# Performance work log

Hardware: AMD Instinct MI355X
Metric: run time of the kernel (lower is better)

## Reference

```python
import jax, jax.numpy as jnp
import numpy as np

BLANK = 0
B, T, D_TN = 32, 1000, 640
D_PN, D_J, V = 640, 640, 1024


def lstm_step(x, h, c, W_ih, W_hh, b):
    # x:[B,D_PN] h,c:[B,D_PN]
    gates = x @ W_ih.T + h @ W_hh.T + b  # [B,4*D_PN]
    i, f, g, o = jnp.split(gates, 4, axis=-1)
    c_new = jax.nn.sigmoid(f) * c + jax.nn.sigmoid(i) * jnp.tanh(g)
    h_new = jax.nn.sigmoid(o) * jnp.tanh(c_new)
    return h_new, c_new


def setup_inputs() -> dict:
    key = jax.random.key(0)
    ks = jax.random.split(key, 10)
    s_pn = 1.0 / np.sqrt(D_PN)
    s_tn = 1.0 / np.sqrt(D_TN)
    s_j = 1.0 / np.sqrt(D_J)
    return {
        "tn_output": jax.random.normal(ks[0], (B, T, D_TN), jnp.float32),
        "E": jax.random.normal(ks[1], (V, D_PN), jnp.float32) * 0.02,
        "W_ih": jax.random.normal(ks[2], (4 * D_PN, D_PN), jnp.float32) * s_pn,
        "W_hh": jax.random.normal(ks[3], (4 * D_PN, D_PN), jnp.float32) * s_pn,
        "b_lstm": jnp.zeros((4 * D_PN,), jnp.float32),
        "W_tn": jax.random.normal(ks[4], (D_J, D_TN), jnp.float32) * s_tn,
        "W_pn": jax.random.normal(ks[5], (D_J, D_PN), jnp.float32) * s_pn,
        "b_joint": jnp.zeros((D_J,), jnp.float32),
        "W_out": jax.random.normal(ks[6], (V, D_J), jnp.float32) * s_j,
        "b_out": jnp.zeros((V,), jnp.float32),
    }


def reference(tn_output, E, W_ih, W_hh, b_lstm, W_tn, W_pn, b_joint, W_out, b_out):
    """Vectorized transducer greedy decode (beam_size=1 path).
    Returns (emitted_tokens [B,T] (blank where no emission), logp_scores [B],
    mean exp score scalar) mirroring the torch module's greedy output."""
    b, t = tn_output.shape[0], tn_output.shape[1]
    dt = tn_output.dtype
    # initial PN step on initial_token_id (= blank), hidden None -> zeros
    h0 = jnp.zeros((b, W_hh.shape[1]), dt)
    c0 = jnp.zeros((b, W_hh.shape[1]), dt)
    x0 = E[jnp.full((b,), BLANK)]
    h, c = lstm_step(x0, h0, c0, W_ih, W_hh, b_lstm)
    out_pn = h
    # precompute TN projection for the whole utterance: [T,B,D_J]
    tn_proj = jnp.einsum("btd,jd->tbj", tn_output, W_tn)

    def step(state, tn_t):
        h, c, out_pn, last_tok, score = state
        z = jnp.tanh(tn_t + out_pn @ W_pn.T + b_joint)          # [B,D_J]
        logp = jax.nn.log_softmax(z @ W_out.T + b_out, axis=-1)  # [B,V]
        pos = jnp.argmax(logp, axis=-1).astype(jnp.int32)        # [B]
        lp = jnp.take_along_axis(logp, pos[:, None].astype(jnp.int32), axis=-1)[:, 0]
        nonblank = pos != BLANK
        score = score + jnp.where(nonblank, lp, jnp.zeros_like(lp))
        tok = jnp.where(nonblank, pos, last_tok)
        # PN advances only for hyps that emitted a non-blank label
        h2, c2 = lstm_step(E[tok], h, c, W_ih, W_hh, b_lstm)
        m = nonblank[:, None]
        h_n = jnp.where(m, h2, h)
        c_n = jnp.where(m, c2, c)
        out_n = jnp.where(m, h2, out_pn)
        emit = jnp.where(nonblank, pos, jnp.full_like(pos, BLANK))
        return (h_n, c_n, out_n, tok, score), emit

    init = (h, c, out_pn, jnp.full((b,), BLANK, jnp.int32), jnp.zeros((b,), dt))
    (_, _, _, _, score), emits = jax.lax.scan(step, init, tn_proj)
    tokens = jnp.swapaxes(emits, 0, 1)  # [B,T]
    return tokens, score, jnp.exp(score).mean()
```

## Files before the change

### kernel.cpp

```cpp
#include <hip/hip_runtime.h>
#include <stdint.h>


typedef unsigned long long u64;
typedef uint32_t u32;

#define TT 1000
#define DD 640
#define GG 2560
#define VV 1024

#define NA 80
#define NL 64
#define NC 80
#define NBLK (NA + NL + NC)

static constexpr size_t OFF_WTN  = 0;
static constexpr size_t OFF_WPN  = OFF_WTN  + 409600;
static constexpr size_t OFF_WHH  = OFF_WPN  + 409600;
static constexpr size_t OFF_WOUT = OFF_WHH  + 1638400;
static constexpr size_t OFF_P    = OFF_WOUT + 655360;
static constexpr size_t OFF_XH   = OFF_P    + 2621440;
static constexpr size_t OFF_XZ   = OFF_XH   + 40960;
static constexpr size_t OFF_SC   = OFF_XZ   + 20480;
static constexpr size_t OFF_LKEY = OFF_SC   + 32;
static constexpr size_t OFF_LSE  = OFF_LKEY + 4096;
static constexpr size_t OFF_FA   = OFF_LSE  + 2048;
static constexpr size_t OFF_FL   = OFF_FA   + 2560;
static constexpr size_t OFF_FC   = OFF_FL   + 2048;
static constexpr size_t OFF_EP   = OFF_FC   + 2560;
static constexpr size_t OFF_END  = OFF_EP   + 96;

__device__ __forceinline__ float sigf(float x) { return 1.0f / (1.0f + expf(-x)); }

__device__ __forceinline__ u32 ordf(float f) {
  u32 u = __float_as_uint(f);
  return (u & 0x80000000u) ? ~u : (u | 0x80000000u);
}

__device__ __forceinline__ void cstore2(float* p, float a, float b) {
  u64 v = ((u64)__float_as_uint(b) << 32) | (u64)__float_as_uint(a);
  __hip_atomic_store((u64*)p, v, __ATOMIC_RELAXED, __HIP_MEMORY_SCOPE_AGENT);
}
__device__ __forceinline__ float2 cload2(const float* p) {
  u64 v = __hip_atomic_load((const u64*)p, __ATOMIC_RELAXED, __HIP_MEMORY_SCOPE_AGENT);
  return make_float2(__uint_as_float((u32)v), __uint_as_float((u32)(v >> 32)));
}
__device__ __forceinline__ u64 cloadu64(const u64* p) {
  return __hip_atomic_load(p, __ATOMIC_RELAXED, __HIP_MEMORY_SCOPE_AGENT);
}
__device__ __forceinline__ void cstoreu64(u64* p, u64 v) {
  __hip_atomic_store(p, v, __ATOMIC_RELAXED, __HIP_MEMORY_SCOPE_AGENT);
}
__device__ __forceinline__ float cloadf(const float* p) {
  return __hip_atomic_load(p, __ATOMIC_RELAXED, __HIP_MEMORY_SCOPE_AGENT);
}
__device__ __forceinline__ void cstoref(float* p, float v) {
  __hip_atomic_store(p, v, __ATOMIC_RELAXED, __HIP_MEMORY_SCOPE_AGENT);
}

__device__ __forceinline__ void poll_flags(const int* F, int n, int target) {
  if ((int)threadIdx.x < n) {
    while (__hip_atomic_load(F + threadIdx.x * 32, __ATOMIC_RELAXED,
                             __HIP_MEMORY_SCOPE_AGENT) < target)
      __builtin_amdgcn_s_sleep(1);
  }
  __syncthreads();
}
__device__ __forceinline__ void poll1(const int* ep, int target) {
  if (threadIdx.x == 0) {
    while (__hip_atomic_load(ep, __ATOMIC_RELAXED, __HIP_MEMORY_SCOPE_AGENT) < target)
      __builtin_amdgcn_s_sleep(1);
  }
  __syncthreads();
}
__device__ __forceinline__ void set_flag(int* F, int idx, int val) {
  __syncthreads();
  if (threadIdx.x == 0)
    __hip_atomic_store(F + idx * 32, val, __ATOMIC_RELAXED, __HIP_MEMORY_SCOPE_AGENT);
}

__device__ __forceinline__ void fma4(float& a, const float4 w, const float4 x) {
  a = fmaf(w.x, x.x, fmaf(w.y, x.y, fmaf(w.z, x.z, fmaf(w.w, x.w, a))));
}
__device__ __forceinline__ void fma22(float& a, const float4 w, const float2 xa,
                                      const float2 xb) {
  a = fmaf(w.x, xa.x, fmaf(w.y, xa.y, fmaf(w.z, xb.x, fmaf(w.w, xb.y, a))));
}


__global__ __launch_bounds__(256) void k_wt4(const float* __restrict__ W,
                                             float* __restrict__ WT4, int J) {
  __shared__ float tile[64][65];
  int nj = J >> 6;
  int tj = blockIdx.x % nj, tk = blockIdx.x / nj;
  int jb = tj << 6, kb = tk << 6;
  for (int i = threadIdx.x; i < 4096; i += 256) {
    int d = i & 63, j = i >> 6;
    tile[j][d] = W[(size_t)(jb + j) * DD + (kb + d)];
  }
  __syncthreads();
  for (int i = threadIdx.x; i < 1024; i += 256) {
    int j = i & 63, q = i >> 6;
    float4 v = make_float4(tile[j][q * 4], tile[j][q * 4 + 1], tile[j][q * 4 + 2],
                           tile[j][q * 4 + 3]);
    ((float4*)WT4)[(size_t)((kb >> 2) + q) * J + (jb + j)] = v;
  }
}

__global__ __launch_bounds__(256) void k_pgemm(const float* __restrict__ E,
                                               const float* __restrict__ Wih,
                                               float* __restrict__ P) {
  __shared__ float As[16][65], Bs[16][65];
  int vt = blockIdx.x & 15, gt = blockIdx.x >> 4;
  int vb = vt << 6, gb = gt << 6;
  int tv = threadIdx.x & 15, tg = threadIdx.x >> 4;
  float acc[4][4] = {};
  for (int kb = 0; kb < DD; kb += 16) {
    for (int i = threadIdx.x; i < 1024; i += 256) {
      int k = i & 15, x = i >> 4;
      As[k][x] = E[(size_t)(vb + x) * DD + kb + k];
      Bs[k][x] = Wih[(size_t)(gb + x) * DD + kb + k];
    }
    __syncthreads();
#pragma unroll
    for (int k = 0; k < 16; ++k) {
      float av[4], bv[4];
#pragma unroll
      for (int i = 0; i < 4; ++i) av[i] = As[k][tv * 4 + i];
#pragma unroll
      for (int j = 0; j < 4; ++j) bv[j] = Bs[k][tg * 4 + j];
#pragma unroll
      for (int i = 0; i < 4; ++i)
#pragma unroll
        for (int j = 0; j < 4; ++j) acc[i][j] = fmaf(av[i], bv[j], acc[i][j]);
    }
    __syncthreads();
  }
#pragma unroll
  for (int i = 0; i < 4; ++i)
#pragma unroll
    for (int j = 0; j < 4; ++j)
      P[(size_t)(vb + tv * 4 + i) * GG + gb + tg * 4 + j] = acc[i][j];
}

__global__ __launch_bounds__(256) void k_init(float* __restrict__ ws,
                                              const float* __restrict__ bl) {
  const float* P = ws + OFF_P;
  float* XH0 = ws + OFF_XH;
  int tid = blockIdx.x * 256 + threadIdx.x;
  if (tid < DD) {
    int j = tid;
    float gi = P[j] + bl[j];
    float gg = P[1280 + j] + bl[1280 + j];
    float go = P[1920 + j] + bl[1920 + j];
    float c1 = sigf(gi) * tanhf(gg);
    float h1 = sigf(go) * tanhf(c1);
    for (int b = 0; b < 32; ++b) XH0[b * DD + j] = h1;
  }
  if (blockIdx.x == 3) {
    int* FA = (int*)(ws + OFF_FA);
    int* FL = (int*)(ws + OFF_FL);
    int* FC = (int*)(ws + OFF_FC);
    int* EP = (int*)(ws + OFF_EP);
    for (int i = threadIdx.x; i < 224; i += 256) {
      int* p = (i < 80) ? (FA + i * 32)
                        : (i < 144) ? (FL + (i - 80) * 32) : (FC + (i - 144) * 32);
      *p = 0;
    }
    if (threadIdx.x < 3) EP[threadIdx.x * 32] = 0;
  }
}

__global__ __launch_bounds__(256, 1) void k_decode(float* __restrict__ ws,
                                                   const float* __restrict__ tn,
                                                   const float* __restrict__ bl,
                                                   const float* __restrict__ bj,
                                                   const float* __restrict__ bo,
                                                   float* __restrict__ out) {
  const float* WTN = ws + OFF_WTN;
  const float* WPN = ws + OFF_WPN;
  const float* WHH = ws + OFF_WHH;
  const float* WOUT = ws + OFF_WOUT;
  const float* P = ws + OFF_P;
  float* XH = ws + OFF_XH;
  float* XZ = ws + OFF_XZ;
  float* SCg = ws + OFF_SC;
  u64* LKEY = (u64*)(ws + OFF_LKEY);
  float* LSE = ws + OFF_LSE;
  int* FA = (int*)(ws + OFF_FA);
  int* FL = (int*)(ws + OFF_FL);
  int* FC = (int*)(ws + OFF_FC);
  int* EFC = (int*)(ws + OFF_EP) + 0;
  int* EFA = (int*)(ws + OFF_EP) + 32;
  int* EFL = (int*)(ws + OFF_EP) + 64;

  __shared__ float xbuf[32 * 648];
  __shared__ float red[16 * 16 * 33];
  __shared__ float aux[32 * 33];
  __shared__ u64 kred[32 * 9];
  __shared__ float sered[32 * 9];
  __shared__ float c_lds[8 * 33], h_lds[8 * 33];
  __shared__ float sc_lds[32];
  __shared__ int tok_lds[32], nb_lds[32], lt_lds[32];

  const int bid = blockIdx.x, tid = threadIdx.x;
  const int dq = tid >> 4, bp = tid & 15;
  const int d0 = dq * 40, b0 = bp * 2;

  if (bid < NA) {
    const int j0 = bid * 8;
    for (int t = 0; t < TT; ++t) {
      const int par = t & 1;
      float acc[8][2] = {};
      const float* t0p = tn + ((size_t)b0 * TT + t) * DD + d0;
      const float* t1p = t0p + (size_t)TT * DD;
#pragma unroll 5
      for (int q = 0; q < 10; ++q) {
        float4 x0 = *(const float4*)(t0p + q * 4);
        float4 x1 = *(const float4*)(t1p + q * 4);
        const float4* wt = (const float4*)WTN + (size_t)((d0 + q * 4) >> 2) * DD + j0;
#pragma unroll
        for (int r = 0; r < 8; ++r) {
          fma4(acc[r][0], wt[r], x0);
          fma4(acc[r][1], wt[r], x1);
        }
      }
      if (bid == 0) {
        poll_flags(FC, NC, t);
        if (tid == 0)
          __hip_atomic_store(EFC, t, __ATOMIC_RELAXED, __HIP_MEMORY_SCOPE_AGENT);
      } else {
        poll1(EFC, t);
      }
      const float* h0p = XH + (size_t)par * 20480 + (size_t)b0 * DD + d0;
      const float* h1p = h0p + DD;
#pragma unroll 5
      for (int q = 0; q < 10; ++q) {
        float2 a0 = cload2(h0p + q * 4), a1 = cload2(h0p + q * 4 + 2);
        float2 b1 = cload2(h1p + q * 4), b2 = cload2(h1p + q * 4 + 2);
        const float4* wp = (const float4*)WPN + (size_t)((d0 + q * 4) >> 2) * DD + j0;
#pragma unroll
        for (int r = 0; r < 8; ++r) {
          fma22(acc[r][0], wp[r], a0, a1);
          fma22(acc[r][1], wp[r], b1, b2);
        }
      }
#pragma unroll
      for (int r = 0; r < 8; ++r) {
        red[(dq * 8 + r) * 33 + b0] = acc[r][0];
        red[(dq * 8 + r) * 33 + b0 + 1] = acc[r][1];
      }
      __syncthreads();
      {
        int r = tid >> 5, b = tid & 31;
        float s = 0.f;
#pragma unroll
        for (int k = 0; k < 16; ++k) s += red[(k * 8 + r) * 33 + b];
        aux[r * 33 + b] = tanhf(s + bj[j0 + r]);
      }
      __syncthreads();
      if (tid < 128) {
        int jp = tid >> 5, b = tid & 31;
        cstore2(XZ + (size_t)b * DD + j0 + jp * 2, aux[(jp * 2) * 33 + b],
                aux[(jp * 2 + 1) * 33 + b]);
      }
      set_flag(FA, bid, t + 1);
    }
  } else if (bid < NA + NL) {
    const int lb = bid - NA, v0 = lb * 16;
    for (int t = 0; t < TT; ++t) {
      if (lb == 0) {
        poll_flags(FA, NA, t + 1);
        if (tid == 0)
          __hip_atomic_store(EFA, t + 1, __ATOMIC_RELAXED, __HIP_MEMORY_SCOPE_AGENT);
      } else {
        poll1(EFA, t + 1);
      }
      const float* z0p = XZ + (size_t)b0 * DD + d0;
      const float* z1p = z0p + DD;
      float acc[16][2] = {};
#pragma unroll 5
      for (int q = 0; q < 10; ++q) {
        float2 z0a = cload2(z0p + q * 4), z0b = cload2(z0p + q * 4 + 2);
        float2 z1a = cload2(z1p + q * 4), z1b = cload2(z1p + q * 4 + 2);
        const float4* wo = (const float4*)WOUT + (size_t)((d0 + q * 4) >> 2) * VV + v0;
#pragma unroll
        for (int r = 0; r < 16; ++r) {
          float4 w = wo[r];
          fma22(acc[r][0], w, z0a, z0b);
          fma22(acc[r][1], w, z1a, z1b);
        }
      }
#pragma unroll
      for (int r = 0; r < 16; ++r) {
        red[(dq * 16 + r) * 33 + b0] = acc[r][0];
        red[(dq * 16 + r) * 33 + b0 + 1] = acc[r][1];
      }
      __syncthreads();
#pragma unroll
      for (int o = tid; o < 512; o += 256) {
        int r = o >> 5, b = o & 31;
        float s = bo[v0 + r];
#pragma unroll
        for (int k = 0; k < 16; ++k) s += red[(k * 16 + r) * 33 + b];
        aux[r * 33 + b] = s;
      }
      __syncthreads();
      if (tid < 32) {
        int b = tid;
        float m = -1e30f, se = 0.f;
        int vbest = 0;
#pragma unroll
        for (int r = 0; r < 16; ++r) {
          float x = aux[r * 33 + b];
          se += expf(x);
          if (x > m) { m = x; vbest = r; }
        }
        u64 key = ((u64)ordf(m) << 32) | (u64)(0xFFFFFFFFu - (u32)(v0 + vbest));
        cstoreu64(&LKEY[(size_t)b * 64 + lb], key);
        cstoref(&LSE[(size_t)b * 64 + lb], se);
      }
      set_flag(FL, lb, t + 1);
    }
  } else {
    const int cb = bid - (NA + NL), j0 = cb * 8;
    {
      int jj = tid >> 5, b = tid & 31, j = j0 + jj;
      float gi = P[j] + bl[j];
      float gg = P[1280 + j] + bl[1280 + j];
      float go = P[1920 + j] + bl[1920 + j];
      float c1 = sigf(gi) * tanhf(gg);
      c_lds[jj * 33 + b] = c1;
      h_lds[jj * 33 + b] = sigf(go) * tanhf(c1);
    }
    if (tid < 32) { lt_lds[tid] = 0; sc_lds[tid] = 0.f; }
    __syncthreads();
    for (int t = 0; t < TT; ++t) {
      const int par = t & 1;
      poll1(EFC, t);
      {
        const float* h0p = XH + (size_t)par * 20480 + (size_t)b0 * DD + d0;
        const float* h1p = h0p + DD;
#pragma unroll 5
        for (int q = 0; q < 10; ++q) {
          float2 a0 = cload2(h0p + q * 4), a1 = cload2(h0p + q * 4 + 2);
          float2 b1 = cload2(h1p + q * 4), b2 = cload2(h1p + q * 4 + 2);
          *(float4*)&xbuf[b0 * 648 + d0 + q * 4] = make_float4(a0.x, a0.y, a1.x, a1.y);
          *(float4*)&xbuf[(b0 + 1) * 648 + d0 + q * 4] = make_float4(b1.x, b1.y, b2.x, b2.y);
        }
      }
      __syncthreads();
#pragma unroll
      for (int p = 0; p < 2; ++p) {
        float acc[16][2] = {};
#pragma unroll 5
        for (int q = 0; q < 10; ++q) {
          const int d = d0 + q * 4;
          float4 h0 = *(const float4*)&xbuf[b0 * 648 + d];
          float4 h1 = *(const float4*)&xbuf[(b0 + 1) * 648 + d];
          const float4* wa =
              (const float4*)WHH + (size_t)(d >> 2) * GG + (2 * p) * DD + j0;
          const float4* wb = wa + DD;
#pragma unroll
          for (int jj = 0; jj < 8; ++jj) {
            fma4(acc[jj][0], wa[jj], h0);
            fma4(acc[jj][1], wa[jj], h1);
            fma4(acc[8 + jj][0], wb[jj], h0);
            fma4(acc[8 + jj][1], wb[jj], h1);
          }
        }
#pragma unroll
        for (int r = 0; r < 16; ++r) {
          red[(dq * 16 + r) * 33 + b0] = acc[r][0];
          red[(dq * 16 + r) * 33 + b0 + 1] = acc[r][1];
        }
        __syncthreads();
#pragma unroll
        for (int o = tid; o < 512; o += 256) {
          int r16 = o >> 5, b = o & 31;
          float s = 0.f;
#pragma unroll
          for (int k = 0; k < 16; ++k) s += red[(k * 16 + r16) * 33 + b];
          int g = 2 * p + (r16 >> 3), jj = r16 & 7;
          aux[(g * 8 + jj) * 33 + b] = s;
        }
        __syncthreads();
      }
      if (cb == 0) {
        poll_flags(FL, NL, t + 1);
        if (tid == 0)
          __hip_atomic_store(EFL, t + 1, __ATOMIC_RELAXED, __HIP_MEMORY_SCOPE_AGENT);
      } else {
        poll1(EFL, t + 1);
      }
      {
        int b = tid >> 3, ch = tid & 7;
        const u64* kp = LKEY + (size_t)b * 64 + ch * 8;
        u64 km = 0;
#pragma unroll
        for (int i = 0; i < 8; ++i) {
          u64 x = cloadu64(kp + i);
          km = x > km ? x : km;
        }
        kred[b * 9 + ch] = km;
        if (cb == 0) {
          const float* sp = LSE + (size_t)b * 64 + ch * 8;
          float ss = 0.f;
#pragma unroll
          for (int i = 0; i < 8; ++i) ss += cloadf(sp + i);
          sered[b * 9 + ch] = ss;
        }
      }
      __syncthreads();
      if (tid < 32) {
        int b = tid;
        u64 km = 0;
#pragma unroll
        for (int ch = 0; ch < 8; ++ch) {
          u64 x = kred[b * 9 + ch];
          km = x > km ? x : km;
        }
        u32 ou = (u32)(km >> 32);
        u32 fb = (ou & 0x80000000u) ? (ou & 0x7FFFFFFFu) : ~ou;
        float m = __uint_as_float(fb);
        int v = (int)(0xFFFFFFFFu - (u32)(km & 0xFFFFFFFFull));
        int nb = (v != 0) ? 1 : 0;
        int tok = nb ? v : lt_lds[b];
        lt_lds[b] = tok;
        tok_lds[b] = tok;
        nb_lds[b] = nb;
        if (cb == 0) {
          float S = 0.f;
#pragma unroll
          for (int ch = 0; ch < 8; ++ch) S += sered[b * 9 + ch];
          float lp = m - logf(S);
          if (nb) sc_lds[b] += lp;
          out[(size_t)b * TT + t] = nb ? (float)v : 0.0f;
          if (t == TT - 1) SCg[b] = sc_lds[b];
        }
      }
      __syncthreads();
      {
        int jj = tid >> 5, b = tid & 31, j = j0 + jj;
        if (nb_lds[b]) {
          const float* Pr = P + (size_t)tok_lds[b] * GG;
          float gi = aux[(0 + jj) * 33 + b] + Pr[j] + bl[j];
          float gf = aux[(8 + jj) * 33 + b] + Pr[640 + j] + bl[640 + j];
          float gg = aux[(16 + jj) * 33 + b] + Pr[1280 + j] + bl[1280 + j];
          float go = aux[(24 + jj) * 33 + b] + Pr[1920 + j] + bl[1920 + j];
          float c = c_lds[jj * 33 + b];
          float cn = sigf(gf) * c + sigf(gi) * tanhf(gg);
          float hn = sigf(go) * tanhf(cn);
          c_lds[jj * 33 + b] = cn;
          h_lds[jj * 33 + b] = hn;
        }
      }
      __syncthreads();
      if (tid < 128) {
        int jp = tid >> 5, b = tid & 31;
        cstore2(XH + (size_t)(1 - par) * 20480 + (size_t)b * DD + j0 + jp * 2,
                h_lds[(jp * 2) * 33 + b], h_lds[(jp * 2 + 1) * 33 + b]);
      }
      set_flag(FC, cb, t + 1);
    }
  }
}

__global__ __launch_bounds__(64) void k_final(const float* __restrict__ ws,
                                              float* __restrict__ out) {
  __shared__ float sh[32];
  int t = threadIdx.x;
  if (t < 32) {
    float s = ws[OFF_SC + t];
    out[32000 + t] = s;
    sh[t] = expf(s);
  }
  __syncthreads();
  if (t == 0) {
    float a = 0.f;
    for (int i = 0; i < 32; ++i) a += sh[i];
    out[32032] = a / 32.0f;
  }
}

extern "C" void kernel_launch(void* const* d_in, const int* in_sizes, int n_in,
                              void* d_out, int out_size, void* d_ws, size_t ws_size,
                              hipStream_t stream) {
  const float* tn = (const float*)d_in[0];
  const float* E = (const float*)d_in[1];
  const float* Wih = (const float*)d_in[2];
  const float* Whh = (const float*)d_in[3];
  const float* bl = (const float*)d_in[4];
  const float* Wtn = (const float*)d_in[5];
  const float* Wpn = (const float*)d_in[6];
  const float* bj = (const float*)d_in[7];
  const float* Wout = (const float*)d_in[8];
  const float* bo = (const float*)d_in[9];
  float* ws = (float*)d_ws;
  float* out = (float*)d_out;

  k_wt4<<<100, 256, 0, stream>>>(Wtn, ws + OFF_WTN, DD);
  k_wt4<<<100, 256, 0, stream>>>(Wpn, ws + OFF_WPN, DD);
  k_wt4<<<400, 256, 0, stream>>>(Whh, ws + OFF_WHH, GG);
  k_wt4<<<160, 256, 0, stream>>>(Wout, ws + OFF_WOUT, VV);
  k_pgemm<<<640, 256, 0, stream>>>(E, Wih, ws + OFF_P);
  k_init<<<4, 256, 0, stream>>>(ws, bl);
  k_decode<<<NBLK, 256, 0, stream>>>(ws, tn, bl, bj, bo, out);
  k_final<<<1, 64, 0, stream>>>(ws, out);
}
```

Baseline: 28.33 ms.

## Replace leader-based epoch flags with per-consumer mailbox flag arrays

Inter-block synchronization in the persistent decode kernel changes from a two-hop scheme to direct producer-to-consumer flags. Before, a leader block polled all producer flags and then published one epoch flag that the other blocks polled. Now each producer writes its step counter into a private slot for every consumer, and each consumer polls its own packed array. This drops one serial polling hop per stage on the critical path of the recurrent loop. In exchange, producers issue many more stores per step, the flag workspace grows, and the poll sleep interval is raised.

```diff
diff --git a/kernel.cpp b/kernel.cpp
--- a/kernel.cpp
+++ b/kernel.cpp
@@ -25,11 +25,10 @@
 static constexpr size_t OFF_SC   = OFF_XZ   + 20480;
 static constexpr size_t OFF_LKEY = OFF_SC   + 32;
 static constexpr size_t OFF_LSE  = OFF_LKEY + 4096;
-static constexpr size_t OFF_FA   = OFF_LSE  + 2048;
-static constexpr size_t OFF_FL   = OFF_FA   + 2560;
-static constexpr size_t OFF_FC   = OFF_FL   + 2048;
-static constexpr size_t OFF_EP   = OFF_FC   + 2560;
-static constexpr size_t OFF_END  = OFF_EP   + 96;
+static constexpr size_t OFF_MCFC = OFF_LSE  + 2048;
+static constexpr size_t OFF_MCFA = OFF_MCFC + 51200;
+static constexpr size_t OFF_MCFL = OFF_MCFA + 20480;
+static constexpr size_t OFF_END  = OFF_MCFL + 20480;
 
 __device__ __forceinline__ float sigf(float x) { return 1.0f / (1.0f + expf(-x)); }
 
@@ -59,25 +58,20 @@
   __hip_atomic_store(p, v, __ATOMIC_RELAXED, __HIP_MEMORY_SCOPE_AGENT);
 }
 
-__device__ __forceinline__ void poll_flags(const int* F, int n, int target) {
-  if ((int)threadIdx.x < n) {
-    while (__hip_atomic_load(F + threadIdx.x * 32, __ATOMIC_RELAXED,
+__device__ __forceinline__ void wait_mc(const int* mc, int nprod, int target) {
+  if ((int)threadIdx.x < nprod) {
+    while (__hip_atomic_load(mc + threadIdx.x * 4, __ATOMIC_RELAXED,
                              __HIP_MEMORY_SCOPE_AGENT) < target)
-      __builtin_amdgcn_s_sleep(1);
+      __builtin_amdgcn_s_sleep(2);
   }
   __syncthreads();
 }
-__device__ __forceinline__ void poll1(const int* ep, int target) {
-  if (threadIdx.x == 0) {
-    while (__hip_atomic_load(ep, __ATOMIC_RELAXED, __HIP_MEMORY_SCOPE_AGENT) < target)
-      __builtin_amdgcn_s_sleep(1);
-  }
+__device__ __forceinline__ void publish_mc(int* mc, int ncons, int nprod,
+                                           int myprod, int val) {
   __syncthreads();
-}
-__device__ __forceinline__ void set_flag(int* F, int idx, int val) {
-  __syncthreads();
-  if (threadIdx.x == 0)
-    __hip_atomic_store(F + idx * 32, val, __ATOMIC_RELAXED, __HIP_MEMORY_SCOPE_AGENT);
+  if ((int)threadIdx.x < ncons)
+    __hip_atomic_store(mc + ((size_t)threadIdx.x * nprod + myprod) * 4, val,
+                       __ATOMIC_RELAXED, __HIP_MEMORY_SCOPE_AGENT);
 }
 
 __device__ __forceinline__ void fma4(float& a, const float4 w, const float4 x) {
@@ -158,18 +152,8 @@
     float h1 = sigf(go) * tanhf(c1);
     for (int b = 0; b < 32; ++b) XH0[b * DD + j] = h1;
   }
-  if (blockIdx.x == 3) {
-    int* FA = (int*)(ws + OFF_FA);
-    int* FL = (int*)(ws + OFF_FL);
-    int* FC = (int*)(ws + OFF_FC);
-    int* EP = (int*)(ws + OFF_EP);
-    for (int i = threadIdx.x; i < 224; i += 256) {
-      int* p = (i < 80) ? (FA + i * 32)
-                        : (i < 144) ? (FL + (i - 80) * 32) : (FC + (i - 144) * 32);
-      *p = 0;
-    }
-    if (threadIdx.x < 3) EP[threadIdx.x * 32] = 0;
-  }
+  int* mc = (int*)(ws + OFF_MCFC);
+  for (int i = tid; i < 92160; i += 1024) mc[i] = 0;
 }
 
 __global__ __launch_bounds__(256, 1) void k_decode(float* __restrict__ ws,
@@ -188,12 +172,9 @@
   float* SCg = ws + OFF_SC;
   u64* LKEY = (u64*)(ws + OFF_LKEY);
   float* LSE = ws + OFF_LSE;
-  int* FA = (int*)(ws + OFF_FA);
-  int* FL = (int*)(ws + OFF_FL);
-  int* FC = (int*)(ws + OFF_FC);
-  int* EFC = (int*)(ws + OFF_EP) + 0;
-  int* EFA = (int*)(ws + OFF_EP) + 32;
-  int* EFL = (int*)(ws + OFF_EP) + 64;
+  int* MCFC = (int*)(ws + OFF_MCFC);
+  int* MCFA = (int*)(ws + OFF_MCFA);
+  int* MCFL = (int*)(ws + OFF_MCFL);
 
   __shared__ float xbuf[32 * 648];
   __shared__ float red[16 * 16 * 33];
@@ -210,6 +191,7 @@
 
   if (bid < NA) {
     const int j0 = bid * 8;
+    const int* myFC = MCFC + (size_t)bid * 320;
     for (int t = 0; t < TT; ++t) {
       const int par = t & 1;
       float acc[8][2] = {};
@@ -226,13 +208,7 @@
           fma4(acc[r][1], wt[r], x1);
         }
       }
-      if (bid == 0) {
-        poll_flags(FC, NC, t);
-        if (tid == 0)
-          __hip_atomic_store(EFC, t, __ATOMIC_RELAXED, __HIP_MEMORY_SCOPE_AGENT);
-      } else {
-        poll1(EFC, t);
-      }
+      wait_mc(myFC, NC, t);
       const float* h0p = XH + (size_t)par * 20480 + (size_t)b0 * DD + d0;
       const float* h1p = h0p + DD;
 #pragma unroll 5
@@ -265,18 +241,13 @@
         cstore2(XZ + (size_t)b * DD + j0 + jp * 2, aux[(jp * 2) * 33 + b],
                 aux[(jp * 2 + 1) * 33 + b]);
       }
-      set_flag(FA, bid, t + 1);
+      publish_mc(MCFA, NL, NA, bid, t + 1);
     }
   } else if (bid < NA + NL) {
     const int lb = bid - NA, v0 = lb * 16;
+    const int* myFA = MCFA + (size_t)lb * 320;
     for (int t = 0; t < TT; ++t) {
-      if (lb == 0) {
-        poll_flags(FA, NA, t + 1);
-        if (tid == 0)
-          __hip_atomic_store(EFA, t + 1, __ATOMIC_RELAXED, __HIP_MEMORY_SCOPE_AGENT);
-      } else {
-        poll1(EFA, t + 1);
-      }
+      wait_mc(myFA, NA, t + 1);
       const float* z0p = XZ + (size_t)b0 * DD + d0;
       const float* z1p = z0p + DD;
       float acc[16][2] = {};
@@ -321,10 +292,12 @@
         cstoreu64(&LKEY[(size_t)b * 64 + lb], key);
         cstoref(&LSE[(size_t)b * 64 + lb], se);
       }
-      set_flag(FL, lb, t + 1);
+      publish_mc(MCFL, NC, NL, lb, t + 1);
     }
   } else {
     const int cb = bid - (NA + NL), j0 = cb * 8;
+    const int* myFC = MCFC + (size_t)(NA + cb) * 320;
+    const int* myFL = MCFL + (size_t)cb * 256;
     {
       int jj = tid >> 5, b = tid & 31, j = j0 + jj;
       float gi = P[j] + bl[j];
@@ -338,7 +311,7 @@
     __syncthreads();
     for (int t = 0; t < TT; ++t) {
       const int par = t & 1;
-      poll1(EFC, t);
+      wait_mc(myFC, NC, t);
       {
         const float* h0p = XH + (size_t)par * 20480 + (size_t)b0 * DD + d0;
         const float* h1p = h0p + DD;
@@ -387,13 +360,7 @@
         }
         __syncthreads();
       }
-      if (cb == 0) {
-        poll_flags(FL, NL, t + 1);
-        if (tid == 0)
-          __hip_atomic_store(EFL, t + 1, __ATOMIC_RELAXED, __HIP_MEMORY_SCOPE_AGENT);
-      } else {
-        poll1(EFL, t + 1);
-      }
+      wait_mc(myFL, NL, t + 1);
       {
         int b = tid >> 3, ch = tid & 7;
         const u64* kp = LKEY + (size_t)b * 64 + ch * 8;
@@ -462,7 +429,7 @@
         cstore2(XH + (size_t)(1 - par) * 20480 + (size_t)b * DD + j0 + jp * 2,
                 h_lds[(jp * 2) * 33 + b], h_lds[(jp * 2 + 1) * 33 + b]);
       }
-      set_flag(FC, cb, t + 1);
+      publish_mc(MCFC, NA + NC, NC, cb, t + 1);
     }
   }
 }
```

Measured after the change: 26.95 ms. 4.9% less time.
